# Performance work log

Hardware: AMD Instinct MI355X
Metric: run time of the kernel (lower is better)

## Reference

```python
import math
import jax, jax.numpy as jnp
import numpy as np

E = 64   # embed_size (also per-head dim)
H = 8    # heads
B = 4
T = 2048


def setup_inputs() -> dict:
    key = jax.random.key(0)
    ks = jax.random.split(key, 8)
    s_in = 1.0 / math.sqrt(E)
    s_out = 1.0 / math.sqrt(H * E)
    return {
        "values": jax.random.normal(ks[0], (B, T, E), dtype=jnp.float32),
        "keys": jax.random.normal(ks[1], (B, T, E), dtype=jnp.float32),
        "queries": jax.random.normal(ks[2], (B, T, E), dtype=jnp.float32),
        # Linear(E, E*H, bias=False) weights, stored as [in, out] for x @ W
        "Wv": jax.random.uniform(ks[3], (E, E * H), jnp.float32, -s_in, s_in),
        "Wk": jax.random.uniform(ks[4], (E, E * H), jnp.float32, -s_in, s_in),
        "Wq": jax.random.uniform(ks[5], (E, E * H), jnp.float32, -s_in, s_in),
        # unifyheads: Linear(H*E, E)
        "Wu": jax.random.uniform(ks[6], (H * E, E), jnp.float32, -s_out, s_out),
        "bu": jax.random.uniform(ks[7], (E,), jnp.float32, -s_out, s_out),
    }


def reference(values, keys, queries, Wv, Wk, Wq, Wu, bu):
    b, t, e = keys.shape
    h = H
    v = (values @ Wv).reshape(b, t, h, e)   # bthe
    k = (keys @ Wk).reshape(b, t, h, e)
    q = (queries @ Wq).reshape(b, t, h, e)
    dot = jnp.einsum('bthe,bihe->bhti', q, k) / math.sqrt(e)  # [b,h,t,i]
    # NOTE: source applies softmax over dim=2 (the query axis t), faithfully kept
    attention = jax.nn.softmax(dot, axis=2)
    out = jnp.einsum('bhtd,bdhe->bthe', attention, v).reshape(b, t, h * e)
    return out @ Wu + bu
```

## Files before the change

### kernel.cpp

```cpp
#include <hip/hip_runtime.h>


typedef __attribute__((ext_vector_type(8))) __bf16 bf16x8;
typedef __attribute__((ext_vector_type(8))) short short8v;
typedef __attribute__((ext_vector_type(8))) unsigned short ushort8;
typedef __attribute__((ext_vector_type(4))) short short4v;
typedef __attribute__((ext_vector_type(4))) float f32x4;
typedef unsigned int uint32;

constexpr int B_ = 4;
constexpr int T_ = 2048;
constexpr int H_ = 8;
constexpr int E_ = 64;
constexpr int BH_ = B_ * H_;
constexpr int SZ_ = 8;
constexpr int NP_ = 2;
constexpr float QSCALE_ = 0.125f * 1.4426950408889634f;

__device__ inline uint32 f2bf1(float f) {
  uint32 u = __builtin_bit_cast(uint32, f);
  return (u + 0x7fffu + ((u >> 16) & 1u)) >> 16;
}
__device__ inline uint32 pk2(float a, float b) {
#if __has_builtin(__builtin_amdgcn_cvt_pk_bf16_f32)
  return __builtin_bit_cast(uint32, __builtin_amdgcn_cvt_pk_bf16_f32(a, b));
#else
  return f2bf1(a) | (f2bf1(b) << 16);
#endif
}
__device__ inline float bf2f(uint32 bits) {
  return __builtin_bit_cast(float, bits << 16);
}
__device__ inline bf16x8 ld8(const unsigned short* p) {
  return __builtin_bit_cast(bf16x8, *(const ushort8*)p);
}
__device__ inline short4v lo4(bf16x8 v) {
  short8v s = __builtin_bit_cast(short8v, v);
  return __builtin_shufflevector(s, s, 0, 1, 2, 3);
}
__device__ inline short4v hi4(bf16x8 v) {
  short8v s = __builtin_bit_cast(short8v, v);
  return __builtin_shufflevector(s, s, 4, 5, 6, 7);
}
#define MFMA16(a, b, c) __builtin_amdgcn_mfma_f32_16x16x32_bf16(a, b, c, 0, 0, 0)
#define EXP2(x) __builtin_amdgcn_exp2f(x)

__device__ inline f32x4 pv_mfma(short4v a, short4v b, f32x4 c) {
#if __has_builtin(__builtin_amdgcn_mfma_f32_16x16x16bf16_1k)
  return __builtin_amdgcn_mfma_f32_16x16x16bf16_1k(a, b, c, 0, 0, 0);
#else
  asm("v_mfma_f32_16x16x16_bf16 %0, %1, %2, %0" : "+v"(c) : "v"(a), "v"(b));
  return c;
#endif
}

__device__ inline void dma16(const unsigned short* g, unsigned short* l) {
  __builtin_amdgcn_global_load_lds(
      (const __attribute__((address_space(1))) void*)g,
      (__attribute__((address_space(3))) void*)l, 16, 0, 0);
}

__global__ __launch_bounds__(512) void proj_kernel(
    const float* __restrict__ Xq, const float* __restrict__ Xk,
    const float* __restrict__ Xv, const float* __restrict__ Wq,
    const float* __restrict__ Wk, const float* __restrict__ Wv,
    unsigned short* __restrict__ Yq, unsigned short* __restrict__ Yk,
    unsigned short* __restrict__ Yv) {
  constexpr int RT = 16;
  __shared__ float xs[RT][E_];
  const int z = blockIdx.y;
  const float* X = (z == 0) ? Xq : (z == 1) ? Xk : Xv;
  const float* W = (z == 0) ? Wq : (z == 1) ? Wk : Wv;
  unsigned short* Y = (z == 0) ? Yq : (z == 1) ? Yk : Yv;
  const float scale = (z == 0) ? QSCALE_ : 1.0f;
  const int row0 = blockIdx.x * RT;
  const int tid = threadIdx.x;
#pragma unroll
  for (int idx = tid; idx < RT * E_; idx += 512)
    xs[idx >> 6][idx & 63] = X[(size_t)(row0 + (idx >> 6)) * E_ + (idx & 63)];
  __syncthreads();
  const int j = tid;
  const int h = j >> 6, e = j & 63;
  float acc[RT];
#pragma unroll
  for (int r = 0; r < RT; ++r) acc[r] = 0.f;
  for (int c = 0; c < E_; ++c) {
    const float w = W[c * (H_ * E_) + j];
#pragma unroll
    for (int r = 0; r < RT; ++r) acc[r] += xs[r][c] * w;
  }
#pragma unroll
  for (int r = 0; r < RT; ++r) {
    const int row = row0 + r;
    const int b = row >> 11, t = row & (T_ - 1);
    Y[(((size_t)(b * H_ + h) * T_ + t) << 6) + e] =
        (unsigned short)f2bf1(acc[r] * scale);
  }
}

__global__ __launch_bounds__(256, 4) void stats_kernel(
    const unsigned short* __restrict__ K16, const unsigned short* __restrict__ Q16,
    float* __restrict__ s_part) {
  const int g = blockIdx.x;
  const int x = g & 7, s = g >> 3;
  const int bh = x + 8 * (s >> 6);
  const int rem = s & 63;
  const int zi = rem >> 3;
  const int dblk = rem & 7;
  const int tid = threadIdx.x;
  const int w = tid >> 6, lane = tid & 63;
  const int lm = lane & 15, lq = lane >> 4;
  const int d0 = dblk * 256 + w * 64;
  const int tz0 = zi * (T_ / SZ_);
  const unsigned short* Kp = K16 + (size_t)bh * T_ * E_;
  const unsigned short* Qp = Q16 + (size_t)bh * T_ * E_;

  bf16x8 kf[4][2];
#pragma unroll
  for (int dt = 0; dt < 4; ++dt) {
    kf[dt][0] = ld8(&Kp[(size_t)(d0 + dt * 16 + lm) * E_ + lq * 8]);
    kf[dt][1] = ld8(&Kp[(size_t)(d0 + dt * 16 + lm) * E_ + 32 + lq * 8]);
  }
  f32x4 sacc[4];
#pragma unroll
  for (int dt = 0; dt < 4; ++dt) sacc[dt] = (f32x4){0.f, 0.f, 0.f, 0.f};
  const f32x4 zero = {0.f, 0.f, 0.f, 0.f};

  for (int t0 = tz0; t0 < tz0 + (T_ / SZ_); t0 += 32) {
    const bf16x8 q0l = ld8(&Qp[(size_t)(t0 + lm) * E_ + lq * 8]);
    const bf16x8 q0h = ld8(&Qp[(size_t)(t0 + lm) * E_ + 32 + lq * 8]);
    const bf16x8 q1l = ld8(&Qp[(size_t)(t0 + 16 + lm) * E_ + lq * 8]);
    const bf16x8 q1h = ld8(&Qp[(size_t)(t0 + 16 + lm) * E_ + 32 + lq * 8]);
#pragma unroll
    for (int dt = 0; dt < 4; ++dt) {
      f32x4 c = MFMA16(kf[dt][0], q0l, zero);
      c = MFMA16(kf[dt][1], q0h, c);
#pragma unroll
      for (int r = 0; r < 4; ++r) sacc[dt][r] += EXP2(c[r]);
    }
#pragma unroll
    for (int dt = 0; dt < 4; ++dt) {
      f32x4 c = MFMA16(kf[dt][0], q1l, zero);
      c = MFMA16(kf[dt][1], q1h, c);
#pragma unroll
      for (int r = 0; r < 4; ++r) sacc[dt][r] += EXP2(c[r]);
    }
  }
#pragma unroll
  for (int m = 1; m < 16; m <<= 1) {
#pragma unroll
    for (int dt = 0; dt < 4; ++dt)
#pragma unroll
      for (int r = 0; r < 4; ++r)
        sacc[dt][r] += __shfl_xor(sacc[dt][r], m);
  }
  if (lm == 0) {
#pragma unroll
    for (int dt = 0; dt < 4; ++dt)
#pragma unroll
      for (int r = 0; r < 4; ++r)
        s_part[((size_t)zi * BH_ + bh) * T_ + d0 + dt * 16 + lq * 4 + r] =
            sacc[dt][r];
  }
}

__global__ __launch_bounds__(256) void scale_kernel(
    const unsigned short* __restrict__ V16, const float* __restrict__ s_part,
    unsigned short* __restrict__ Vt16) {
  __shared__ float ts[64][68];
  __shared__ float sinv_s[64];
  const int bh = blockIdx.y;
  const int d0 = blockIdx.x * 64;
  const unsigned short* Vp = V16 + (size_t)bh * T_ * E_;
  const int tid = threadIdx.x;
  if (tid < 64) {
    float s = 0.f;
#pragma unroll
    for (int z = 0; z < SZ_; ++z)
      s += s_part[((size_t)z * BH_ + bh) * T_ + d0 + tid];
    sinv_s[tid] = 1.0f / s;
  }
  __syncthreads();
  for (int idx = tid; idx < 64 * 8; idx += 256) {
    const int r = idx >> 3, c8 = idx & 7;
    const ushort8 v8 = *(const ushort8*)&Vp[(size_t)(d0 + r) * E_ + c8 * 8];
    const float is = sinv_s[r];
#pragma unroll
    for (int k = 0; k < 8; ++k) ts[r][c8 * 8 + k] = bf2f(v8[k]) * is;
  }
  __syncthreads();
  for (int idx = tid; idx < 64 * 16; idx += 256) {
    const int e = idx >> 4, q = idx & 15;
    float v[4];
#pragma unroll
    for (int j = 0; j < 4; ++j) {
      const int pos = q * 4 + j;
      const int c32 = pos >> 5, i = pos & 31;
      const int lqp = i >> 3, u = i & 7;
      const int dl = (u < 4) ? (lqp * 4 + u) : (16 + lqp * 4 + (u - 4));
      v[j] = ts[c32 * 32 + dl][e];
    }
    uint2 o = make_uint2(pk2(v[0], v[1]), pk2(v[2], v[3]));
    *(uint2*)&Vt16[((size_t)bh * E_ + e) * T_ + d0 + q * 4] = o;
  }
}

__global__ __launch_bounds__(256, 4) void apply_kernel(
    const unsigned short* __restrict__ K16, const unsigned short* __restrict__ Q16,
    const unsigned short* __restrict__ Vt16, float* __restrict__ o_part) {
  __shared__ __align__(16) unsigned short K_s[2][64 * 64];
  __shared__ __align__(16) unsigned short V_s[2][64 * 64];
  const int g = blockIdx.x;
  const int xcd = g & 7, slot = g >> 3;
  const int bh = xcd + 8 * (slot >> 5);
  const int rem = slot & 31;
  const int np = rem >> 4;
  const int tblk = rem & 15;
  const int b = bh >> 3, h = bh & 7;
  const int tid = threadIdx.x;
  const int w = tid >> 6, lane = tid & 63;
  const int lm = lane & 15, lq = lane >> 4;
  const int t0 = tblk * 128 + w * 32;
  const int dbase = np * (T_ / NP_);
  constexpr int NC = (T_ / NP_) / 64;
  const unsigned short* Kp = K16 + (size_t)bh * T_ * E_;
  const unsigned short* Qp = Q16 + (size_t)bh * T_ * E_;
  const unsigned short* Vp = Vt16 + (size_t)bh * E_ * T_;

  const int kr = lane >> 3, kp = lane & 7;
  const unsigned short* gK = Kp + (size_t)(w * 16 + kr) * E_ + (kp ^ kr) * 8;
  const unsigned short* gV = Vp + (size_t)(w * 16 + kr) * T_ + kp * 8;
  unsigned short* lK0 = &K_s[0][w * 1024];
  unsigned short* lK1 = &K_s[1][w * 1024];
  unsigned short* lV0 = &V_s[0][w * 1024];
  unsigned short* lV1 = &V_s[1][w * 1024];

  bf16x8 qf[2][2];
#pragma unroll
  for (int tt = 0; tt < 2; ++tt) {
    qf[tt][0] = ld8(&Qp[(size_t)(t0 + tt * 16 + lm) * E_ + lq * 8]);
    qf[tt][1] = ld8(&Qp[(size_t)(t0 + tt * 16 + lm) * E_ + 32 + lq * 8]);
  }
  f32x4 acc[2][4];
#pragma unroll
  for (int tt = 0; tt < 2; ++tt)
#pragma unroll
    for (int ec = 0; ec < 4; ++ec) acc[tt][ec] = (f32x4){0.f, 0.f, 0.f, 0.f};
  const f32x4 zero = {0.f, 0.f, 0.f, 0.f};

  dma16(gK + (size_t)dbase * E_, lK0);
  dma16(gK + (size_t)dbase * E_ + 8 * E_, lK0 + 512);
  dma16(gV + dbase, lV0);
  dma16(gV + dbase + 8 * T_, lV0 + 512);
  __syncthreads();

  for (int c = 0; c < NC; ++c) {
    const int cur = c & 1;
    const unsigned short* Kb = K_s[cur];
    const unsigned short* Vb = V_s[cur];
    bf16x8 kf[4][2];
#pragma unroll
    for (int dd = 0; dd < 4; ++dd)
#pragma unroll
      for (int hi = 0; hi < 2; ++hi)
        kf[dd][hi] =
            ld8(&Kb[(dd * 16 + lm) * 64 + (((hi * 4 + lq) ^ (lm & 7)) * 8)]);
    bf16x8 vf[2][4];
#pragma unroll
    for (int h2 = 0; h2 < 2; ++h2)
#pragma unroll
      for (int ec = 0; ec < 4; ++ec)
        vf[h2][ec] = ld8(&Vb[(ec * 16 + lm) * 64 + h2 * 32 + lq * 8]);
    if (c + 1 < NC) {
      const int dn = dbase + (c + 1) * 64;
      unsigned short* nK = cur ? lK0 : lK1;
      unsigned short* nV = cur ? lV0 : lV1;
      dma16(gK + (size_t)dn * E_, nK);
      dma16(gK + (size_t)dn * E_ + 8 * E_, nK + 512);
      dma16(gV + dn, nV);
      dma16(gV + dn + 8 * T_, nV + 512);
    }
#pragma unroll
    for (int h2 = 0; h2 < 2; ++h2) {
#pragma unroll
      for (int tt = 0; tt < 2; ++tt) {
        f32x4 c0 = MFMA16(kf[2 * h2][0], qf[tt][0], zero);
        c0 = MFMA16(kf[2 * h2][1], qf[tt][1], c0);
        f32x4 c1 = MFMA16(kf[2 * h2 + 1][0], qf[tt][0], zero);
        c1 = MFMA16(kf[2 * h2 + 1][1], qf[tt][1], c1);
        const uint32 b00 = pk2(EXP2(c0[0]), EXP2(c0[1]));
        const uint32 b01 = pk2(EXP2(c0[2]), EXP2(c0[3]));
        const uint32 b10 = pk2(EXP2(c1[0]), EXP2(c1[1]));
        const uint32 b11 = pk2(EXP2(c1[2]), EXP2(c1[3]));
        const short4v eB0 = __builtin_bit_cast(short4v, make_uint2(b00, b01));
        const short4v eB1 = __builtin_bit_cast(short4v, make_uint2(b10, b11));
#pragma unroll
        for (int ec = 0; ec < 4; ++ec) {
          acc[tt][ec] = pv_mfma(lo4(vf[h2][ec]), eB0, acc[tt][ec]);
          acc[tt][ec] = pv_mfma(hi4(vf[h2][ec]), eB1, acc[tt][ec]);
        }
      }
    }
    __syncthreads();
  }

  float* op_base = o_part + (size_t)np * BH_ * T_ * E_;
#pragma unroll
  for (int tt = 0; tt < 2; ++tt) {
    const int t = t0 + tt * 16 + lm;
#pragma unroll
    for (int ec = 0; ec < 4; ++ec) {
      float* op = &op_base[((size_t)(b * T_ + t) * H_ + h) * E_ + ec * 16 + lq * 4];
      *(float4*)op = make_float4(acc[tt][ec][0], acc[tt][ec][1],
                                 acc[tt][ec][2], acc[tt][ec][3]);
    }
  }
}

__global__ __launch_bounds__(256) void unify_kernel(
    const float* __restrict__ o0, const float* __restrict__ o1,
    const float* __restrict__ Wu, const float* __restrict__ bu,
    float* __restrict__ out) {
  constexpr int RT = 16;
  __shared__ float xs[RT][H_ * E_];
  const int row0 = blockIdx.x * RT;
  const int tid = threadIdx.x;
  for (int idx = tid; idx < RT * 128; idx += 256) {
    const int r = idx >> 7, c4 = idx & 127;
    const float4 a = *(const float4*)&o0[(size_t)(row0 + r) * 512 + c4 * 4];
    const float4 bv = *(const float4*)&o1[(size_t)(row0 + r) * 512 + c4 * 4];
    xs[r][c4 * 4 + 0] = a.x + bv.x;
    xs[r][c4 * 4 + 1] = a.y + bv.y;
    xs[r][c4 * 4 + 2] = a.z + bv.z;
    xs[r][c4 * 4 + 3] = a.w + bv.w;
  }
  __syncthreads();
  const int j = tid & 63;
  const int rg = tid >> 6;
  float acc[4] = {0.f, 0.f, 0.f, 0.f};
  for (int c = 0; c < 512; ++c) {
    const float w = Wu[c * 64 + j];
#pragma unroll
    for (int r = 0; r < 4; ++r) acc[r] += xs[rg * 4 + r][c] * w;
  }
  const float bias = bu[j];
#pragma unroll
  for (int r = 0; r < 4; ++r)
    out[(size_t)(row0 + rg * 4 + r) * 64 + j] = acc[r] + bias;
}

extern "C" void kernel_launch(void* const* d_in, const int* in_sizes, int n_in,
                              void* d_out, int out_size, void* d_ws, size_t ws_size,
                              hipStream_t stream) {
  const float* values  = (const float*)d_in[0];
  const float* keys    = (const float*)d_in[1];
  const float* queries = (const float*)d_in[2];
  const float* Wv      = (const float*)d_in[3];
  const float* Wk      = (const float*)d_in[4];
  const float* Wq      = (const float*)d_in[5];
  const float* Wu      = (const float*)d_in[6];
  const float* bu      = (const float*)d_in[7];
  float* out = (float*)d_out;

  const size_t NQ = (size_t)BH_ * T_ * E_;
  unsigned short* q_bf  = (unsigned short*)d_ws;
  unsigned short* k_bf  = q_bf + NQ;
  unsigned short* v_bf  = k_bf + NQ;
  unsigned short* vt_bf = v_bf + NQ;
  float* o_ws   = (float*)(vt_bf + NQ);
  float* s_part = o_ws + (size_t)NP_ * NQ;

  proj_kernel<<<dim3(B_ * T_ / 16, 3), 512, 0, stream>>>(
      queries, keys, values, Wq, Wk, Wv, q_bf, k_bf, v_bf);
  stats_kernel<<<T_ / 256 * BH_ * SZ_, 256, 0, stream>>>(k_bf, q_bf, s_part);
  scale_kernel<<<dim3(T_ / 64, BH_), 256, 0, stream>>>(v_bf, s_part, vt_bf);
  apply_kernel<<<BH_ * (T_ / 128) * NP_, 256, 0, stream>>>(k_bf, q_bf, vt_bf, o_ws);
  unify_kernel<<<B_ * T_ / 16, 256, 0, stream>>>(o_ws, o_ws + NQ, Wu, bu, out);
}
```

Baseline: 274.2 us.

## Stage Q tile in swizzled LDS and double per-wave K columns in stats kernel

The stats kernel now copies its 256-row Q slice into XOR-swizzled shared memory once per block, and each wave reads Q fragments from LDS instead of global memory. Each wave also keeps 128 key columns (8 K fragments) resident instead of 64, so every Q fragment load feeds twice as many MFMAs. The grid is halved to 1024 blocks to match. This cuts redundant global Q traffic and raises MFMA reuse, at the cost of more registers, 32KB of LDS per block and fewer blocks, which may lower occupancy.

```diff
diff --git a/kernel.cpp b/kernel.cpp
--- a/kernel.cpp
+++ b/kernel.cpp
@@ -101,62 +101,67 @@
 __global__ __launch_bounds__(256, 4) void stats_kernel(
     const unsigned short* __restrict__ K16, const unsigned short* __restrict__ Q16,
     float* __restrict__ s_part) {
+  __shared__ __align__(16) unsigned short Q_s[256 * 64];
   const int g = blockIdx.x;
-  const int x = g & 7, s = g >> 3;
-  const int bh = x + 8 * (s >> 6);
-  const int rem = s & 63;
-  const int zi = rem >> 3;
-  const int dblk = rem & 7;
+  const int xcd = g & 7, slot = g >> 3;
+  const int bh = xcd + 8 * (slot >> 5);
+  const int rem = slot & 31;
+  const int zi = rem >> 2;
+  const int dblk = rem & 3;
   const int tid = threadIdx.x;
   const int w = tid >> 6, lane = tid & 63;
   const int lm = lane & 15, lq = lane >> 4;
-  const int d0 = dblk * 256 + w * 64;
+  const int d0 = dblk * 512 + w * 128;
   const int tz0 = zi * (T_ / SZ_);
   const unsigned short* Kp = K16 + (size_t)bh * T_ * E_;
   const unsigned short* Qp = Q16 + (size_t)bh * T_ * E_;
 
-  bf16x8 kf[4][2];
-#pragma unroll
-  for (int dt = 0; dt < 4; ++dt) {
-    kf[dt][0] = ld8(&Kp[(size_t)(d0 + dt * 16 + lm) * E_ + lq * 8]);
-    kf[dt][1] = ld8(&Kp[(size_t)(d0 + dt * 16 + lm) * E_ + 32 + lq * 8]);
-  }
-  f32x4 sacc[4];
-#pragma unroll
-  for (int dt = 0; dt < 4; ++dt) sacc[dt] = (f32x4){0.f, 0.f, 0.f, 0.f};
+  {
+    const unsigned short* src = &Qp[(size_t)(tz0 + tid) * E_];
+    ushort8 seg[8];
+#pragma unroll
+    for (int s2 = 0; s2 < 8; ++s2) seg[s2] = *(const ushort8*)&src[s2 * 8];
+#pragma unroll
+    for (int s2 = 0; s2 < 8; ++s2)
+      *(ushort8*)&Q_s[tid * 64 + ((s2 ^ (tid & 7)) * 8)] = seg[s2];
+  }
+
+  bf16x8 kf[8][2];
+#pragma unroll
+  for (int dt = 0; dt < 8; ++dt)
+#pragma unroll
+    for (int hi = 0; hi < 2; ++hi)
+      kf[dt][hi] = ld8(&Kp[(size_t)(d0 + dt * 16 + lm) * E_ + hi * 32 + lq * 8]);
+
+  f32x4 sacc[8];
+#pragma unroll
+  for (int dt = 0; dt < 8; ++dt) sacc[dt] = (f32x4){0.f, 0.f, 0.f, 0.f};
   const f32x4 zero = {0.f, 0.f, 0.f, 0.f};
 
-  for (int t0 = tz0; t0 < tz0 + (T_ / SZ_); t0 += 32) {
-    const bf16x8 q0l = ld8(&Qp[(size_t)(t0 + lm) * E_ + lq * 8]);
-    const bf16x8 q0h = ld8(&Qp[(size_t)(t0 + lm) * E_ + 32 + lq * 8]);
-    const bf16x8 q1l = ld8(&Qp[(size_t)(t0 + 16 + lm) * E_ + lq * 8]);
-    const bf16x8 q1h = ld8(&Qp[(size_t)(t0 + 16 + lm) * E_ + 32 + lq * 8]);
-#pragma unroll
-    for (int dt = 0; dt < 4; ++dt) {
-      f32x4 c = MFMA16(kf[dt][0], q0l, zero);
-      c = MFMA16(kf[dt][1], q0h, c);
+  __syncthreads();
+
+  for (int t0 = 0; t0 < 256; t0 += 16) {
+    const bf16x8 q0 = ld8(&Q_s[(t0 + lm) * 64 + ((lq ^ (lm & 7)) * 8)]);
+    const bf16x8 q1 = ld8(&Q_s[(t0 + lm) * 64 + (((4 + lq) ^ (lm & 7)) * 8)]);
+#pragma unroll
+    for (int dt = 0; dt < 8; ++dt) {
+      f32x4 c = MFMA16(kf[dt][0], q0, zero);
+      c = MFMA16(kf[dt][1], q1, c);
 #pragma unroll
       for (int r = 0; r < 4; ++r) sacc[dt][r] += EXP2(c[r]);
     }
-#pragma unroll
-    for (int dt = 0; dt < 4; ++dt) {
-      f32x4 c = MFMA16(kf[dt][0], q1l, zero);
-      c = MFMA16(kf[dt][1], q1h, c);
-#pragma unroll
-      for (int r = 0; r < 4; ++r) sacc[dt][r] += EXP2(c[r]);
-    }
   }
 #pragma unroll
   for (int m = 1; m < 16; m <<= 1) {
 #pragma unroll
-    for (int dt = 0; dt < 4; ++dt)
+    for (int dt = 0; dt < 8; ++dt)
 #pragma unroll
       for (int r = 0; r < 4; ++r)
         sacc[dt][r] += __shfl_xor(sacc[dt][r], m);
   }
   if (lm == 0) {
 #pragma unroll
-    for (int dt = 0; dt < 4; ++dt)
+    for (int dt = 0; dt < 8; ++dt)
 #pragma unroll
       for (int r = 0; r < 4; ++r)
         s_part[((size_t)zi * BH_ + bh) * T_ + d0 + dt * 16 + lq * 4 + r] =
@@ -372,7 +377,7 @@
 
   proj_kernel<<<dim3(B_ * T_ / 16, 3), 512, 0, stream>>>(
       queries, keys, values, Wq, Wk, Wv, q_bf, k_bf, v_bf);
-  stats_kernel<<<T_ / 256 * BH_ * SZ_, 256, 0, stream>>>(k_bf, q_bf, s_part);
+  stats_kernel<<<1024, 256, 0, stream>>>(k_bf, q_bf, s_part);
   scale_kernel<<<dim3(T_ / 64, BH_), 256, 0, stream>>>(v_bf, s_part, vt_bf);
   apply_kernel<<<BH_ * (T_ / 128) * NP_, 256, 0, stream>>>(k_bf, q_bf, vt_bf, o_ws);
   unify_kernel<<<B_ * T_ / 16, 256, 0, stream>>>(o_ws, o_ws + NQ, Wu, bu, out);
```

After: 414.0 us. +51.0%, slower.
